# Kernel tuning notes

Hardware: AMD Instinct MI355X
Metric: run time of the kernel (lower is better)

Reference implementation:

```python
import math
import jax, jax.numpy as jnp
import numpy as np

NUM_BUCKETS = 32
MAX_DISTANCE = 128
N_HEADS = 16
D_KV = 64


def _relative_position_bucket(rel_pos, num_buckets=NUM_BUCKETS, max_distance=MAX_DISTANCE):
    # bidirectional=True branch of T5's bucketing
    num_buckets = num_buckets // 2
    rel_buckets = (rel_pos > 0).astype(jnp.int32) * num_buckets
    rel_pos = jnp.abs(rel_pos)
    max_exact = num_buckets // 2
    is_small = rel_pos < max_exact
    # safe log (values < max_exact are masked out by is_small)
    rp_f = jnp.maximum(rel_pos, 1).astype(jnp.float32)
    rel_if_large = max_exact + (
        jnp.log(rp_f / max_exact) / math.log(max_distance / max_exact) * (num_buckets - max_exact)
    ).astype(jnp.int32)
    rel_if_large = jnp.minimum(rel_if_large, num_buckets - 1)
    return rel_buckets + jnp.where(is_small, rel_pos, rel_if_large)


def compute_bias(rel_bias_table, q_len, k_len):
    ctx = jnp.arange(q_len)[:, None]
    mem = jnp.arange(k_len)[None, :]
    buckets = _relative_position_bucket(mem - ctx)  # [q, k]
    values = rel_bias_table[buckets]                # [q, k, h]
    return jnp.transpose(values, (2, 0, 1))[None]   # [1, h, q, k]


def setup_inputs() -> dict:
    key = jax.random.key(0)
    k1, k2, k3, k4 = jax.random.split(key, 4)
    d_model = 1024
    return {
        "hidden_states": jax.random.normal(k1, (2, 2048, d_model), jnp.float32),
        "w_qkv": jax.random.normal(k2, (d_model, 3 * N_HEADS * D_KV), jnp.float32) * (d_model ** -0.5),
        "w_o": jax.random.normal(k3, (N_HEADS * D_KV, d_model), jnp.float32) * ((N_HEADS * D_KV) ** -0.5),
        "rel_bias_table": jax.random.normal(k4, (NUM_BUCKETS, N_HEADS), jnp.float32),
    }


def reference(hidden_states, w_qkv, w_o, rel_bias_table):
    b, s, _ = hidden_states.shape
    inner = N_HEADS * D_KV
    qkv = hidden_states @ w_qkv                         # [b, s, 3*inner]
    q, k, v = jnp.split(qkv, [inner, 2 * inner], axis=-1)
    def to_bhsd(x):
        return jnp.transpose(x.reshape(b, s, N_HEADS, D_KV), (0, 2, 1, 3))
    q, k, v = to_bhsd(q), to_bhsd(k), to_bhsd(v)
    scores = jnp.einsum("bhqd,bhkd->bhqk", q, k)        # no 1/sqrt(d) scaling in T5
    position_bias = compute_bias(rel_bias_table, s, s)  # [1, h, q, k]
    scores = scores + position_bias
    attn = jax.nn.softmax(scores.astype(jnp.float32), axis=-1).astype(scores.dtype)
    out = jnp.einsum("bhqk,bhkd->bhqd", attn, v)
    out = jnp.transpose(out, (0, 2, 1, 3)).reshape(b, s, inner)
    attn_output = out @ w_o
    return attn_output, position_bias
```

## Files before the change

kernel.cpp:

```cpp
#include <hip/hip_runtime.h>
#include <hip/hip_bf16.h>
#include <cstdint>
#include <cstddef>

#define S_LEN 2048
#define NH 16
#define DKV 64
#define BATCH 2
#define DMODEL 1024
#define LOG2E 1.4426950408889634f

typedef _Float16 half_t;
typedef __attribute__((ext_vector_type(4))) _Float16 halfx4;
typedef __attribute__((ext_vector_type(8))) _Float16 half8;
typedef __attribute__((ext_vector_type(4))) float floatx4;

__device__ __forceinline__ void load_lds16(const half_t* g, half_t* l) {
  __builtin_amdgcn_global_load_lds((const __attribute__((address_space(1))) void*)g,
                                   (__attribute__((address_space(3))) void*)l, 16, 0, 0);
}

__device__ __forceinline__ int t5_bucket(int delta) {
  int base = (delta > 0) ? 16 : 0;
  int a = delta < 0 ? -delta : delta;
  int n;
  if (a < 8)       n = a;
  else if (a < 12) n = 8;
  else if (a < 16) n = 9;
  else if (a < 23) n = 10;
  else if (a < 32) n = 11;
  else if (a < 46) n = 12;
  else if (a < 64) n = 13;
  else if (a < 91) n = 14;
  else             n = 15;
  return base + n;
}

__global__ __launch_bounds__(256) void bias_kernel(const float* __restrict__ table,
                                                   float* __restrict__ out) {
  int h = blockIdx.x >> 11;
  int q = blockIdx.x & (S_LEN - 1);
  __shared__ float tb[32];
  if (threadIdx.x < 32) tb[threadIdx.x] = table[threadIdx.x * NH + h];
  __syncthreads();
  float* dst = out + (size_t)blockIdx.x * S_LEN;
  int k0 = threadIdx.x * 4;
#pragma unroll
  for (int half = 0; half < 2; half++) {
    int k = k0 + half * 1024;
    floatx4 v;
    v[0] = tb[t5_bucket((k + 0) - q)];
    v[1] = tb[t5_bucket((k + 1) - q)];
    v[2] = tb[t5_bucket((k + 2) - q)];
    v[3] = tb[t5_bucket((k + 3) - q)];
    __builtin_nontemporal_store(v, (floatx4*)(dst + k));
  }
}

__global__ __launch_bounds__(256) void cast_f2h(const float* __restrict__ in,
                                                half_t* __restrict__ out) {
  int i = blockIdx.x * 256 + threadIdx.x;
  float4 v = ((const float4*)in)[i];
  halfx4 h;
  h[0] = (half_t)v.x; h[1] = (half_t)v.y; h[2] = (half_t)v.z; h[3] = (half_t)v.w;
  ((halfx4*)out)[i] = h;
}

__global__ __launch_bounds__(256) void transpose_cast(const float* __restrict__ in,
                                                      half_t* __restrict__ out,
                                                      int R, int C) {
  __shared__ float t[32][33];
  int lr = threadIdx.x >> 3;
  int lc = (threadIdx.x & 7) * 4;
  int r0 = blockIdx.y * 32, c0 = blockIdx.x * 32;
  float4 v = *(const float4*)(in + (size_t)(r0 + lr) * C + c0 + lc);
  t[lr][lc + 0] = v.x; t[lr][lc + 1] = v.y; t[lr][lc + 2] = v.z; t[lr][lc + 3] = v.w;
  __syncthreads();
  halfx4 hv;
#pragma unroll
  for (int u = 0; u < 4; u++) hv[u] = (half_t)t[lc + u][lr];
  *(halfx4*)(out + (size_t)(c0 + lr) * R + r0 + lc) = hv;
}

__global__ __launch_bounds__(256) void vtrans(const half_t* __restrict__ V,
                                              half_t* __restrict__ Vt) {
  __shared__ half_t T[64 * 72];
  const int bh = blockIdx.y;
  const int s0 = blockIdx.x * 64;
  const half_t* src = V + ((size_t)bh * S_LEN + s0) * DKV;
  half_t* dst = Vt + (size_t)bh * DKV * S_LEN + s0;
  const int sr = threadIdx.x >> 3;
  const int dc = (threadIdx.x & 7) * 8;
#pragma unroll
  for (int p = 0; p < 2; p++) {
    int s = sr + p * 32;
    half8 v = *(const half8*)(src + (size_t)s * DKV + dc);
#pragma unroll
    for (int u = 0; u < 8; u++) T[(dc + u) * 72 + s] = v[u];
  }
  __syncthreads();
#pragma unroll
  for (int p = 0; p < 2; p++) {
    int d = sr + p * 32;
    half8 v = *(half8*)&T[d * 72 + dc];
    *(half8*)(dst + (size_t)d * S_LEN + dc) = v;
  }
}

template <int MODE>
__global__ __launch_bounds__(256) void hgemm128(const half_t* __restrict__ A,
                                                const half_t* __restrict__ Bt,
                                                float* __restrict__ C,
                                                half_t* __restrict__ Qo,
                                                half_t* __restrict__ Ko,
                                                half_t* __restrict__ Vo,
                                                int M, int N, int K) {
  __shared__ half_t Asl[8 * 1024];
  __shared__ half_t Bsl[8 * 1024];

  const int tid = threadIdx.x;
  const int w = tid >> 6;
  const int lane = tid & 63;
  const int l15 = lane & 15;
  const int quad = lane >> 4;
  const int wm = w >> 1, wn = w & 1;
  const int m0 = blockIdx.y * 128;
  const int n0 = blockIdx.x * 128;

  floatx4 acc[4][4];
#pragma unroll
  for (int i = 0; i < 4; i++)
#pragma unroll
    for (int j = 0; j < 4; j++) acc[i][j] = (floatx4){0.f, 0.f, 0.f, 0.f};

  const half_t* ga0 = A + (size_t)(m0 + (2 * w + 0) * 16 + l15) * K + quad * 8;
  const half_t* ga1 = A + (size_t)(m0 + (2 * w + 1) * 16 + l15) * K + quad * 8;
  const half_t* gb0 = Bt + (size_t)(n0 + (2 * w + 0) * 16 + l15) * K + quad * 8;
  const half_t* gb1 = Bt + (size_t)(n0 + (2 * w + 1) * 16 + l15) * K + quad * 8;
  half_t* la0 = &Asl[(2 * w + 0) * 1024];
  half_t* la1 = &Asl[(2 * w + 1) * 1024];
  half_t* lb0 = &Bsl[(2 * w + 0) * 1024];
  half_t* lb1 = &Bsl[(2 * w + 1) * 1024];

  for (int k0 = 0; k0 < K; k0 += 64) {
    __syncthreads();
    load_lds16(ga0 + k0,      la0);
    load_lds16(ga0 + k0 + 32, la0 + 512);
    load_lds16(ga1 + k0,      la1);
    load_lds16(ga1 + k0 + 32, la1 + 512);
    load_lds16(gb0 + k0,      lb0);
    load_lds16(gb0 + k0 + 32, lb0 + 512);
    load_lds16(gb1 + k0,      lb1);
    load_lds16(gb1 + k0 + 32, lb1 + 512);
    __syncthreads();

#pragma unroll
    for (int ks = 0; ks < 2; ks++) {
      half8 af[4], bf[4];
#pragma unroll
      for (int i = 0; i < 4; i++)
        af[i] = *(half8*)&Asl[(wm * 4 + i) * 1024 + ks * 512 + lane * 8];
#pragma unroll
      for (int j = 0; j < 4; j++)
        bf[j] = *(half8*)&Bsl[(wn * 4 + j) * 1024 + ks * 512 + lane * 8];
#pragma unroll
      for (int i = 0; i < 4; i++)
#pragma unroll
        for (int j = 0; j < 4; j++)
          acc[i][j] = __builtin_amdgcn_mfma_f32_16x16x32_f16(bf[j], af[i], acc[i][j], 0, 0, 0);
    }
  }

  const int rowbase = m0 + wm * 64;
  const int colbase = n0 + wn * 64;
  if (MODE == 0) {
#pragma unroll
    for (int i = 0; i < 4; i++)
#pragma unroll
      for (int j = 0; j < 4; j++)
        *(floatx4*)&C[(size_t)(rowbase + i * 16 + l15) * N + colbase + j * 16 + quad * 4] =
            acc[i][j];
  } else {
    const int which = colbase >> 10;
    const int h = (colbase & 1023) >> 6;
    const int b = rowbase >> 11;
    const int s0 = rowbase & (S_LEN - 1);
    const float scale = (which == 0) ? LOG2E : 1.0f;
    half_t* base = ((which == 0) ? Qo : (which == 1) ? Ko : Vo) +
                   (size_t)(b * NH + h) * S_LEN * DKV;
#pragma unroll
    for (int i = 0; i < 4; i++)
#pragma unroll
      for (int j = 0; j < 4; j++) {
        halfx4 hv;
#pragma unroll
        for (int r = 0; r < 4; r++) hv[r] = (half_t)(acc[i][j][r] * scale);
        *(halfx4*)&base[(size_t)(s0 + i * 16 + l15) * DKV + j * 16 + quad * 4] = hv;
      }
  }
}

__global__ __launch_bounds__(512) void attn_fused(const half_t* __restrict__ Q,
                                                  const half_t* __restrict__ K,
                                                  const half_t* __restrict__ Vt,
                                                  const float* __restrict__ table,
                                                  half_t* __restrict__ X) {
  __shared__ half_t Ks[64 * 64];
  __shared__ half_t Vts[64 * 64];
  __shared__ float tb[32];
  __shared__ float badd2[344];

  const int tid = threadIdx.x;
  const int w = tid >> 6;
  const int lane = tid & 63;
  const int l15 = lane & 15;
  const int quad = lane >> 4;
  const int bh = blockIdx.y;
  const int h = bh & (NH - 1);
  const int q0w = blockIdx.x * 128 + w * 16;

  if (tid < 32) tb[tid] = table[tid * NH + h] * LOG2E;
  __syncthreads();
  if (tid < 337) badd2[tid] = tb[t5_bucket(tid - 168)];
  const float tb_neg = tb[15], tb_pos = tb[31];

  half8 qf[2];
#pragma unroll
  for (int ks = 0; ks < 2; ks++)
    qf[ks] = *(const half8*)(Q + ((size_t)bh * S_LEN + q0w + l15) * DKV +
                             ks * 32 + quad * 8);

  floatx4 o[4];
#pragma unroll
  for (int nb = 0; nb < 4; nb++) o[nb] = (floatx4){0.f, 0.f, 0.f, 0.f};
  float m = -1e30f, l = 0.0f;

  const int jr = tid >> 3;
  const int u = tid & 7;
  const int swu = (u ^ (jr & 7)) * 8;
  const int kv_rd0 = l15 * 64 + ((0 * 4 + quad) ^ (l15 & 7)) * 8;
  const int kv_rd1 = l15 * 64 + ((1 * 4 + quad) ^ (l15 & 7)) * 8;
  const int q2h = quad >> 1, q2l = (quad & 1) * 4;

  const half_t* Kg = K + ((size_t)bh * S_LEN + jr) * DKV + u * 8;
  const half_t* Vg = Vt + ((size_t)bh * DKV + jr) * S_LEN + u * 8;
  int rel = -q0w;

  half8 kreg = *(const half8*)Kg;
  half8 vreg = *(const half8*)Vg;

  for (int it = 0; it < 32; it++, rel += 64) {
    __syncthreads();
    *(half8*)&Ks[jr * 64 + swu] = kreg;
    *(half8*)&Vts[jr * 64 + swu] = vreg;
    __syncthreads();
    if (it < 31) {
      Kg += 64 * DKV;
      Vg += 64;
      kreg = *(const half8*)Kg;
      vreg = *(const half8*)Vg;
    }

    const bool capped = (rel >= 106 || rel <= -154);
    floatx4 s[4];
    if (capped) {
#pragma unroll
      for (int nb = 0; nb < 4; nb++) s[nb] = (floatx4){0.f, 0.f, 0.f, 0.f};
    } else {
      const int db = rel + quad * 4 - l15 + 168;
#pragma unroll
      for (int nb = 0; nb < 4; nb++) {
        s[nb][0] = badd2[db + nb * 16 + 0];
        s[nb][1] = badd2[db + nb * 16 + 1];
        s[nb][2] = badd2[db + nb * 16 + 2];
        s[nb][3] = badd2[db + nb * 16 + 3];
      }
    }
#pragma unroll
    for (int nb = 0; nb < 4; nb++) {
      s[nb] = __builtin_amdgcn_mfma_f32_16x16x32_f16(
          *(half8*)&Ks[nb * 1024 + kv_rd0], qf[0], s[nb], 0, 0, 0);
      s[nb] = __builtin_amdgcn_mfma_f32_16x16x32_f16(
          *(half8*)&Ks[nb * 1024 + kv_rd1], qf[1], s[nb], 0, 0, 0);
    }

    float cm = fmaxf(fmaxf(fmaxf(s[0][0], s[0][1]), fmaxf(s[0][2], s[0][3])),
                     fmaxf(fmaxf(s[1][0], s[1][1]), fmaxf(s[1][2], s[1][3])));
    cm = fmaxf(cm, fmaxf(fmaxf(fmaxf(s[2][0], s[2][1]), fmaxf(s[2][2], s[2][3])),
                         fmaxf(fmaxf(s[3][0], s[3][1]), fmaxf(s[3][2], s[3][3]))));
    {
      int i = __builtin_amdgcn_ds_swizzle(__float_as_int(cm), 0x401F);
      cm = fmaxf(cm, __int_as_float(i));
      cm = fmaxf(cm, __shfl_xor(cm, 32));
    }
    if (!__all(cm <= m)) {
      float mn = fmaxf(m, cm);
      float al = exp2f(m - mn);
      l *= al;
#pragma unroll
      for (int nb = 0; nb < 4; nb++)
#pragma unroll
        for (int r = 0; r < 4; r++) o[nb][r] *= al;
      m = mn;
    }

    float lsum = 0.0f;
    halfx4 pvb[4];
    if (capped) {
      const float sh = ((rel >= 106) ? tb_pos : tb_neg) - m;
#pragma unroll
      for (int nb = 0; nb < 4; nb++)
#pragma unroll
        for (int r = 0; r < 4; r++) {
          float p = exp2f(s[nb][r] + sh);
          lsum += p;
          pvb[nb][r] = (half_t)p;
        }
    } else {
#pragma unroll
      for (int nb = 0; nb < 4; nb++)
#pragma unroll
        for (int r = 0; r < 4; r++) {
          float p = exp2f(s[nb][r] - m);
          lsum += p;
          pvb[nb][r] = (half_t)p;
        }
    }
    l += lsum;

#pragma unroll
    for (int nb = 0; nb < 4; nb++) {
      const int vrow = (nb * 16 + l15);
      const int vsw = vrow & 7;
#pragma unroll
      for (int kt = 0; kt < 4; kt++) {
        halfx4 vf = *(halfx4*)&Vts[vrow * 64 + ((kt * 2 + q2h) ^ vsw) * 8 + q2l];
        o[nb] = __builtin_amdgcn_mfma_f32_16x16x16f16(vf, pvb[kt], o[nb], 0, 0, 0);
      }
    }
  }

  {
    int i = __builtin_amdgcn_ds_swizzle(__float_as_int(l), 0x401F);
    l += __int_as_float(i);
    l += __shfl_xor(l, 32);
    const float inv = 1.0f / l;
    const int b = bh >> 4;
    half_t* xp = X + (size_t)(b * S_LEN + q0w + l15) * DMODEL + h * DKV;
#pragma unroll
    for (int nb = 0; nb < 4; nb++) {
      halfx4 hv;
#pragma unroll
      for (int r = 0; r < 4; r++) hv[r] = (half_t)(o[nb][r] * inv);
      *(halfx4*)(xp + nb * 16 + quad * 4) = hv;
    }
  }
}

extern "C" void kernel_launch(void* const* d_in, const int* in_sizes, int n_in,
                              void* d_out, int out_size, void* d_ws, size_t ws_size,
                              hipStream_t stream) {
  const float* hidden = (const float*)d_in[0];
  const float* w_qkv = (const float*)d_in[1];
  const float* w_o = (const float*)d_in[2];
  const float* table = (const float*)d_in[3];

  float* attn_out = (float*)d_out;
  float* bias_out = (float*)d_out + 4194304;

  half_t* Ah  = (half_t*)d_ws;
  half_t* Wqt = Ah + 4194304;
  half_t* Wot = Wqt + 3145728;
  half_t* Qh  = Wot + 1048576;
  half_t* Kh  = Qh + 4194304;
  half_t* Vh  = Kh + 4194304;
  half_t* Xh  = Vh + 4194304;
  half_t* Vth = Ah;

  cast_f2h<<<4096, 256, 0, stream>>>(hidden, Ah);
  transpose_cast<<<dim3(3072 / 32, 1024 / 32), 256, 0, stream>>>(w_qkv, Wqt, 1024, 3072);
  transpose_cast<<<dim3(1024 / 32, 1024 / 32), 256, 0, stream>>>(w_o, Wot, 1024, 1024);
  bias_kernel<<<NH * S_LEN, 256, 0, stream>>>(table, bias_out);

  hgemm128<1><<<dim3(3072 / 128, 4096 / 128), 256, 0, stream>>>(
      Ah, Wqt, nullptr, Qh, Kh, Vh, 4096, 3072, 1024);

  vtrans<<<dim3(S_LEN / 64, BATCH * NH), 256, 0, stream>>>(Vh, Vth);

  attn_fused<<<dim3(S_LEN / 128, BATCH * NH), 512, 0, stream>>>(
      Qh, Kh, Vth, table, Xh);

  hgemm128<0><<<dim3(1024 / 128, 4096 / 128), 256, 0, stream>>>(
      Xh, Wot, attn_out, nullptr, nullptr, nullptr, 4096, 1024, 1024);
}
```

Before: 477.5 us.

## Merge prep kernels and process two KV tiles per attention barrier

Replaces the four setup launches (bias fill, hidden cast, two weight transposes) with a single prep_all kernel that picks its job from the block index, removing launch gaps. The attention loop now stages 128 keys per barrier pair using doubled LDS buffers, which halves the number of synchronisations. The bias lookup table is stored as phase-shifted float4 rows so each tile loads bias in vector reads. Probabilities are packed to fp16 with cvt_pkrtz, which rounds toward zero, and the capped and uncapped exponent paths are merged into one. The larger LDS footprint may reduce occupancy, and the rounding mode differs slightly from the old conversion.

```diff
diff --git a/kernel.cpp b/kernel.cpp
--- a/kernel.cpp
+++ b/kernel.cpp
@@ -11,6 +11,8 @@
 #define LOG2E 1.4426950408889634f
 
 typedef _Float16 half_t;
+typedef __attribute__((ext_vector_type(2))) __fp16 fp16x2;
+typedef __attribute__((ext_vector_type(4))) __fp16 fp16x4;
 typedef __attribute__((ext_vector_type(4))) _Float16 halfx4;
 typedef __attribute__((ext_vector_type(8))) _Float16 half8;
 typedef __attribute__((ext_vector_type(4))) float floatx4;
@@ -36,50 +38,65 @@
   return base + n;
 }
 
-__global__ __launch_bounds__(256) void bias_kernel(const float* __restrict__ table,
-                                                   float* __restrict__ out) {
-  int h = blockIdx.x >> 11;
-  int q = blockIdx.x & (S_LEN - 1);
-  __shared__ float tb[32];
-  if (threadIdx.x < 32) tb[threadIdx.x] = table[threadIdx.x * NH + h];
-  __syncthreads();
-  float* dst = out + (size_t)blockIdx.x * S_LEN;
-  int k0 = threadIdx.x * 4;
-#pragma unroll
-  for (int half = 0; half < 2; half++) {
-    int k = k0 + half * 1024;
-    floatx4 v;
-    v[0] = tb[t5_bucket((k + 0) - q)];
-    v[1] = tb[t5_bucket((k + 1) - q)];
-    v[2] = tb[t5_bucket((k + 2) - q)];
-    v[3] = tb[t5_bucket((k + 3) - q)];
-    __builtin_nontemporal_store(v, (floatx4*)(dst + k));
-  }
-}
-
-__global__ __launch_bounds__(256) void cast_f2h(const float* __restrict__ in,
-                                                half_t* __restrict__ out) {
-  int i = blockIdx.x * 256 + threadIdx.x;
-  float4 v = ((const float4*)in)[i];
-  halfx4 h;
-  h[0] = (half_t)v.x; h[1] = (half_t)v.y; h[2] = (half_t)v.z; h[3] = (half_t)v.w;
-  ((halfx4*)out)[i] = h;
-}
-
-__global__ __launch_bounds__(256) void transpose_cast(const float* __restrict__ in,
-                                                      half_t* __restrict__ out,
-                                                      int R, int C) {
-  __shared__ float t[32][33];
-  int lr = threadIdx.x >> 3;
-  int lc = (threadIdx.x & 7) * 4;
-  int r0 = blockIdx.y * 32, c0 = blockIdx.x * 32;
-  float4 v = *(const float4*)(in + (size_t)(r0 + lr) * C + c0 + lc);
-  t[lr][lc + 0] = v.x; t[lr][lc + 1] = v.y; t[lr][lc + 2] = v.z; t[lr][lc + 3] = v.w;
-  __syncthreads();
-  halfx4 hv;
-#pragma unroll
-  for (int u = 0; u < 4; u++) hv[u] = (half_t)t[lc + u][lr];
-  *(halfx4*)(out + (size_t)(c0 + lr) * R + r0 + lc) = hv;
+__global__ __launch_bounds__(256) void prep_all(const float* __restrict__ hidden,
+                                                const float* __restrict__ w_qkv,
+                                                const float* __restrict__ w_o,
+                                                const float* __restrict__ table,
+                                                half_t* __restrict__ Ah,
+                                                half_t* __restrict__ Wqt,
+                                                half_t* __restrict__ Wot,
+                                                float* __restrict__ bias_out) {
+  __shared__ float smem[32 * 33];
+  const int id = blockIdx.x;
+  const int tid = threadIdx.x;
+
+  if (id < 32768) {
+    const int h = id >> 11;
+    const int q = id & (S_LEN - 1);
+    if (tid < 32) smem[tid] = table[tid * NH + h];
+    __syncthreads();
+    float* dst = bias_out + (size_t)id * S_LEN;
+    const int k0 = tid * 4;
+#pragma unroll
+    for (int hf = 0; hf < 2; hf++) {
+      int k = k0 + hf * 1024;
+      floatx4 v;
+      v[0] = smem[t5_bucket((k + 0) - q)];
+      v[1] = smem[t5_bucket((k + 1) - q)];
+      v[2] = smem[t5_bucket((k + 2) - q)];
+      v[3] = smem[t5_bucket((k + 3) - q)];
+      __builtin_nontemporal_store(v, (floatx4*)(dst + k));
+    }
+  } else if (id < 36864) {
+    const int i = (id - 32768) * 256 + tid;
+    float4 v = ((const float4*)hidden)[i];
+    halfx4 hv;
+    hv[0] = (half_t)v.x; hv[1] = (half_t)v.y; hv[2] = (half_t)v.z; hv[3] = (half_t)v.w;
+    ((halfx4*)Ah)[i] = hv;
+  } else {
+    const float* in;
+    half_t* out;
+    int R, C, bx, by;
+    if (id < 39936) {
+      int t = id - 36864; bx = t % 96; by = t / 96;
+      in = w_qkv; out = Wqt; R = 1024; C = 3072;
+    } else {
+      int t = id - 39936; bx = t & 31; by = t >> 5;
+      in = w_o; out = Wot; R = 1024; C = 1024;
+    }
+    float (*t33)[33] = (float(*)[33])smem;
+    const int lr = tid >> 3;
+    const int lc = (tid & 7) * 4;
+    const int r0 = by * 32, c0 = bx * 32;
+    float4 v = *(const float4*)(in + (size_t)(r0 + lr) * C + c0 + lc);
+    t33[lr][lc + 0] = v.x; t33[lr][lc + 1] = v.y;
+    t33[lr][lc + 2] = v.z; t33[lr][lc + 3] = v.w;
+    __syncthreads();
+    halfx4 hv;
+#pragma unroll
+    for (int u = 0; u < 4; u++) hv[u] = (half_t)t33[lc + u][lr];
+    *(halfx4*)(out + (size_t)(c0 + lr) * R + r0 + lc) = hv;
+  }
 }
 
 __global__ __launch_bounds__(256) void vtrans(const half_t* __restrict__ V,
@@ -205,10 +222,10 @@
                                                   const half_t* __restrict__ Vt,
                                                   const float* __restrict__ table,
                                                   half_t* __restrict__ X) {
-  __shared__ half_t Ks[64 * 64];
-  __shared__ half_t Vts[64 * 64];
+  __shared__ half_t Ks[2 * 64 * 64];
+  __shared__ half_t Vts[2 * 64 * 64];
   __shared__ float tb[32];
-  __shared__ float badd2[344];
+  __shared__ floatx4 badd4[352];
 
   const int tid = threadIdx.x;
   const int w = tid >> 6;
@@ -221,7 +238,17 @@
 
   if (tid < 32) tb[tid] = table[tid * NH + h] * LOG2E;
   __syncthreads();
-  if (tid < 337) badd2[tid] = tb[t5_bucket(tid - 168)];
+  if (tid < 352) {
+    const int p = tid / 88, t = tid - p * 88;
+    floatx4 v;
+#pragma unroll
+    for (int e = 0; e < 4; e++) {
+      int lin = p + 4 * t + e;
+      if (lin > 343) lin = 343;
+      v[e] = tb[t5_bucket(lin - 168)];
+    }
+    badd4[tid] = v;
+  }
   const float tb_neg = tb[15], tb_pos = tb[31];
 
   half8 qf[2];
@@ -246,96 +273,101 @@
   const half_t* Vg = Vt + ((size_t)bh * DKV + jr) * S_LEN + u * 8;
   int rel = -q0w;
 
-  half8 kreg = *(const half8*)Kg;
-  half8 vreg = *(const half8*)Vg;
-
-  for (int it = 0; it < 32; it++, rel += 64) {
-    __syncthreads();
-    *(half8*)&Ks[jr * 64 + swu] = kreg;
-    *(half8*)&Vts[jr * 64 + swu] = vreg;
-    __syncthreads();
-    if (it < 31) {
-      Kg += 64 * DKV;
-      Vg += 64;
-      kreg = *(const half8*)Kg;
-      vreg = *(const half8*)Vg;
-    }
-
-    const bool capped = (rel >= 106 || rel <= -154);
-    floatx4 s[4];
-    if (capped) {
-#pragma unroll
-      for (int nb = 0; nb < 4; nb++) s[nb] = (floatx4){0.f, 0.f, 0.f, 0.f};
-    } else {
-      const int db = rel + quad * 4 - l15 + 168;
+  half8 kreg0 = *(const half8*)Kg;
+  half8 kreg1 = *(const half8*)(Kg + 64 * DKV);
+  half8 vreg0 = *(const half8*)Vg;
+  half8 vreg1 = *(const half8*)(Vg + 64);
+
+  for (int it = 0; it < 16; it++, rel += 128) {
+    __syncthreads();
+    *(half8*)&Ks[jr * 64 + swu] = kreg0;
+    *(half8*)&Ks[4096 + jr * 64 + swu] = kreg1;
+    *(half8*)&Vts[jr * 64 + swu] = vreg0;
+    *(half8*)&Vts[4096 + jr * 64 + swu] = vreg1;
+    __syncthreads();
+    if (it < 15) {
+      Kg += 128 * DKV;
+      Vg += 128;
+      kreg0 = *(const half8*)Kg;
+      kreg1 = *(const half8*)(Kg + 64 * DKV);
+      vreg0 = *(const half8*)Vg;
+      vreg1 = *(const half8*)(Vg + 64);
+    }
+
+#pragma unroll
+    for (int hb = 0; hb < 2; hb++) {
+      const int relh = rel + hb * 64;
+      const half_t* Kb = &Ks[hb * 4096];
+      const half_t* Vb = &Vts[hb * 4096];
+
+      const bool capped = (relh >= 106 || relh <= -154);
+      floatx4 s[4];
+      if (capped) {
+#pragma unroll
+        for (int nb = 0; nb < 4; nb++) s[nb] = (floatx4){0.f, 0.f, 0.f, 0.f};
+      } else {
+        const int db = relh + quad * 4 - l15 + 168;
+        const int ph = db & 3;
+        const int bb = db >> 2;
+#pragma unroll
+        for (int nb = 0; nb < 4; nb++) s[nb] = badd4[ph * 88 + bb + nb * 4];
+      }
 #pragma unroll
       for (int nb = 0; nb < 4; nb++) {
-        s[nb][0] = badd2[db + nb * 16 + 0];
-        s[nb][1] = badd2[db + nb * 16 + 1];
-        s[nb][2] = badd2[db + nb * 16 + 2];
-        s[nb][3] = badd2[db + nb * 16 + 3];
-      }
-    }
-#pragma unroll
-    for (int nb = 0; nb < 4; nb++) {
-      s[nb] = __builtin_amdgcn_mfma_f32_16x16x32_f16(
-          *(half8*)&Ks[nb * 1024 + kv_rd0], qf[0], s[nb], 0, 0, 0);
-      s[nb] = __builtin_amdgcn_mfma_f32_16x16x32_f16(
-          *(half8*)&Ks[nb * 1024 + kv_rd1], qf[1], s[nb], 0, 0, 0);
-    }
-
-    float cm = fmaxf(fmaxf(fmaxf(s[0][0], s[0][1]), fmaxf(s[0][2], s[0][3])),
-                     fmaxf(fmaxf(s[1][0], s[1][1]), fmaxf(s[1][2], s[1][3])));
-    cm = fmaxf(cm, fmaxf(fmaxf(fmaxf(s[2][0], s[2][1]), fmaxf(s[2][2], s[2][3])),
-                         fmaxf(fmaxf(s[3][0], s[3][1]), fmaxf(s[3][2], s[3][3]))));
-    {
-      int i = __builtin_amdgcn_ds_swizzle(__float_as_int(cm), 0x401F);
-      cm = fmaxf(cm, __int_as_float(i));
-      cm = fmaxf(cm, __shfl_xor(cm, 32));
-    }
-    if (!__all(cm <= m)) {
-      float mn = fmaxf(m, cm);
-      float al = exp2f(m - mn);
-      l *= al;
-#pragma unroll
-      for (int nb = 0; nb < 4; nb++)
-#pragma unroll
-        for (int r = 0; r < 4; r++) o[nb][r] *= al;
-      m = mn;
-    }
-
-    float lsum = 0.0f;
-    halfx4 pvb[4];
-    if (capped) {
-      const float sh = ((rel >= 106) ? tb_pos : tb_neg) - m;
-#pragma unroll
-      for (int nb = 0; nb < 4; nb++)
-#pragma unroll
-        for (int r = 0; r < 4; r++) {
-          float p = exp2f(s[nb][r] + sh);
-          lsum += p;
-          pvb[nb][r] = (half_t)p;
+        s[nb] = __builtin_amdgcn_mfma_f32_16x16x32_f16(
+            *(half8*)&Kb[nb * 1024 + kv_rd0], qf[0], s[nb], 0, 0, 0);
+        s[nb] = __builtin_amdgcn_mfma_f32_16x16x32_f16(
+            *(half8*)&Kb[nb * 1024 + kv_rd1], qf[1], s[nb], 0, 0, 0);
+      }
+
+      float c0 = fmaxf(fmaxf(s[0][0], s[0][1]), s[0][2]);
+      float c1 = fmaxf(fmaxf(s[0][3], s[1][0]), s[1][1]);
+      float c2 = fmaxf(fmaxf(s[1][2], s[1][3]), s[2][0]);
+      float c3 = fmaxf(fmaxf(s[2][1], s[2][2]), s[2][3]);
+      float c4 = fmaxf(fmaxf(s[3][0], s[3][1]), s[3][2]);
+      float cm = fmaxf(fmaxf(fmaxf(c0, c1), c2), fmaxf(fmaxf(c3, c4), s[3][3]));
+      {
+        int i = __builtin_amdgcn_ds_swizzle(__float_as_int(cm), 0x401F);
+        cm = fmaxf(cm, __int_as_float(i));
+        cm = fmaxf(cm, __shfl_xor(cm, 32));
+      }
+      if (!__all(cm <= m)) {
+        float mn = fmaxf(m, cm);
+        float al = exp2f(m - mn);
+        l *= al;
+#pragma unroll
+        for (int nb = 0; nb < 4; nb++)
+#pragma unroll
+          for (int r = 0; r < 4; r++) o[nb][r] *= al;
+        m = mn;
+      }
+
+      const float add = capped ? (((relh >= 106) ? tb_pos : tb_neg) - m) : (-m);
+      float lsum = 0.0f;
+      halfx4 pvb[4];
+#pragma unroll
+      for (int nb = 0; nb < 4; nb++) {
+        float p0 = exp2f(s[nb][0] + add);
+        float p1 = exp2f(s[nb][1] + add);
+        float p2 = exp2f(s[nb][2] + add);
+        float p3 = exp2f(s[nb][3] + add);
+        lsum += (p0 + p1) + (p2 + p3);
+        fp16x2 a01 = __builtin_amdgcn_cvt_pkrtz(p0, p1);
+        fp16x2 a23 = __builtin_amdgcn_cvt_pkrtz(p2, p3);
+        fp16x4 a = __builtin_shufflevector(a01, a23, 0, 1, 2, 3);
+        pvb[nb] = __builtin_bit_cast(halfx4, a);
+      }
+      l += lsum;
+
+#pragma unroll
+      for (int nb = 0; nb < 4; nb++) {
+        const int vrow = (nb * 16 + l15);
+        const int vsw = vrow & 7;
+#pragma unroll
+        for (int kt = 0; kt < 4; kt++) {
+          halfx4 vf = *(halfx4*)&Vb[vrow * 64 + ((kt * 2 + q2h) ^ vsw) * 8 + q2l];
+          o[nb] = __builtin_amdgcn_mfma_f32_16x16x16f16(vf, pvb[kt], o[nb], 0, 0, 0);
         }
-    } else {
-#pragma unroll
-      for (int nb = 0; nb < 4; nb++)
-#pragma unroll
-        for (int r = 0; r < 4; r++) {
-          float p = exp2f(s[nb][r] - m);
-          lsum += p;
-          pvb[nb][r] = (half_t)p;
-        }
-    }
-    l += lsum;
-
-#pragma unroll
-    for (int nb = 0; nb < 4; nb++) {
-      const int vrow = (nb * 16 + l15);
-      const int vsw = vrow & 7;
-#pragma unroll
-      for (int kt = 0; kt < 4; kt++) {
-        halfx4 vf = *(halfx4*)&Vts[vrow * 64 + ((kt * 2 + q2h) ^ vsw) * 8 + q2l];
-        o[nb] = __builtin_amdgcn_mfma_f32_16x16x16f16(vf, pvb[kt], o[nb], 0, 0, 0);
       }
     }
   }
@@ -377,10 +409,8 @@
   half_t* Xh  = Vh + 4194304;
   half_t* Vth = Ah;
 
-  cast_f2h<<<4096, 256, 0, stream>>>(hidden, Ah);
-  transpose_cast<<<dim3(3072 / 32, 1024 / 32), 256, 0, stream>>>(w_qkv, Wqt, 1024, 3072);
-  transpose_cast<<<dim3(1024 / 32, 1024 / 32), 256, 0, stream>>>(w_o, Wot, 1024, 1024);
-  bias_kernel<<<NH * S_LEN, 256, 0, stream>>>(table, bias_out);
+  prep_all<<<40960, 256, 0, stream>>>(hidden, w_qkv, w_o, table,
+                                      Ah, Wqt, Wot, bias_out);
 
   hgemm128<1><<<dim3(3072 / 128, 4096 / 128), 256, 0, stream>>>(
       Ah, Wqt, nullptr, Qh, Kh, Vh, 4096, 3072, 1024);
```

Result: no change. 469.0 us (-1.8%).
